# Kernel tuning notes

Hardware: AMD Instinct MI355X
Metric: run time of the kernel (lower is better)

The kernel has to match this reference:

```python
import jax, jax.numpy as jnp
import numpy as np
from jax import lax

BITS = 8
STRIDE = 1
PADDING = 1
SCALE = 2.0 ** (BITS - 1)  # fixed-point scale 2^(bits-1)


def setup_inputs() -> dict:
    key = jax.random.key(0)
    k1, k2, k3 = jax.random.split(key, 3)
    x = jax.random.normal(k1, (32, 128, 56, 56), dtype=jnp.float32)
    W = jax.random.normal(k2, (256, 128, 3, 3), dtype=jnp.float32)
    b = jax.random.normal(k3, (256,), dtype=jnp.float32)
    return {"x": x, "W": W, "b": b}


def reference(x, W, b):
    # to_fix_point: round(v * 2^(bits-1)); torch keeps long ints, but all
    # arithmetic in forward promotes back to float, so float round is exact here.
    w_q = jnp.round(W * SCALE)
    b_q = jnp.round(b * SCALE)
    # calConv: out[i,j] = sum(patch * w_q) / 2^(bits-1) + b_q
    # (square 3x3 kernel makes the original's transposed patch indexing a standard conv)
    out = lax.conv_general_dilated(
        x, w_q,
        window_strides=(STRIDE, STRIDE),
        padding=[(PADDING, PADDING), (PADDING, PADDING)],
        dimension_numbers=("NCHW", "OIHW", "NCHW"),
    )
    return out / SCALE + b_q[None, :, None, None]
```

## Files before the change

### kernel.cpp

```cpp
#include <hip/hip_runtime.h>

typedef _Float16 half8 __attribute__((ext_vector_type(8)));
typedef float floatx4 __attribute__((ext_vector_type(4)));

#define IMG   3136
#define PIMG  3364
#define XP_ELEMS (32 * 58 * 58 * 128)
#define WQ_ELEMS (9 * 256 * 128)

#define AS1 __attribute__((address_space(1)))
#define AS3 __attribute__((address_space(3)))

__global__ __launch_bounds__(256) void pad_x_kernel(const float* __restrict__ x,
                                                    _Float16* __restrict__ xp) {
    const int hh = blockIdx.x;
    const int n  = blockIdx.y;
    const int t  = threadIdx.x;
    _Float16* rowbase = xp + ((long)(n * 58 + hh) * 58) * 128;

    if (hh == 0 || hh == 57) {
        #pragma unroll
        for (int i = 0; i < 4; ++i) {
            int idx = i * 256 + t;
            if (idx < 928) *(half8*)(rowbase + idx * 8) = (half8)(_Float16)0.0f;
        }
        return;
    }

    __shared__ _Float16 tile[128 * 57];
    const int h = hh - 1;

    #pragma unroll
    for (int p = 0; p < 7; ++p) {
        int idx = p * 256 + t;
        int c   = idx / 14;
        int w4  = (idx % 14) * 4;
        const float4 v = *(const float4*)(x + ((long)(n * 128 + c) * 56 + h) * 56 + w4);
        _Float16* d = tile + c * 57 + w4;
        d[0] = (_Float16)v.x; d[1] = (_Float16)v.y;
        d[2] = (_Float16)v.z; d[3] = (_Float16)v.w;
    }
    __syncthreads();

    #pragma unroll
    for (int p = 0; p < 4; ++p) {
        int idx = p * 256 + t;
        if (idx < 896) {
            int ww = idx >> 4;
            int c0 = (idx & 15) * 8;
            half8 v;
            #pragma unroll
            for (int j = 0; j < 8; ++j) v[j] = tile[(c0 + j) * 57 + ww];
            *(half8*)(rowbase + (ww + 1) * 128 + c0) = v;
        }
    }
    if (t < 32) {
        int ww = (t >> 4) ? 57 : 0;
        int c0 = (t & 15) * 8;
        *(half8*)(rowbase + ww * 128 + c0) = (half8)(_Float16)0.0f;
    }
}

__global__ void quant_w_kernel(const float* __restrict__ W, _Float16* __restrict__ wq) {
    int t = blockIdx.x * 256 + threadIdx.x;
    int c  = t & 127;
    int k  = (t >> 7) & 255;
    int rs = t >> 15;
    wq[t] = (_Float16)rintf(W[(k * 128 + c) * 9 + rs] * 128.0f);
}

__global__ __launch_bounds__(256) void conv_mfma_kernel(
    const _Float16* __restrict__ xp, const _Float16* __restrict__ wq,
    const float* __restrict__ b, float* __restrict__ out)
{
    __shared__ __align__(16) _Float16 smem[24576];

    const int tid = threadIdx.x;
    const int l   = tid & 63;
    const int wv  = tid >> 6;
    const int wm  = wv & 1;
    const int wn  = wv >> 1;
    const int bx  = blockIdx.x;

    const int lrow = l >> 2;
    const int lch  = ((l & 3) ^ ((l >> 3) & 3)) * 8;

    int aoff[4];
    #pragma unroll
    for (int i = 0; i < 4; ++i)
        aoff[i] = (i * 64 + wv * 16 + lrow) * 128 + lch;

    int pb[2];
    #pragma unroll
    for (int j = 0; j < 2; ++j) {
        const int pix = bx * 128 + j * 64 + wv * 16 + lrow;
        const int n  = pix / IMG, hw = pix % IMG;
        pb[j] = (n * PIMG + (hw / 56) * 58 + (hw % 56)) * 128 + lch;
    }

    const int stA = wv * 512;

    floatx4 acc[8][4] = {};

    auto issue = [&](int t, int pbuf) {
        const int rs = t >> 2;
        const int cc = t & 3;
        const int r  = (rs * 11) >> 5;
        const int s2 = rs - r * 3;
        const _Float16* wg = wq + rs * (256 * 128) + cc * 32;
        const _Float16* xg = xp + (r * 58 + s2) * 128 + cc * 32;
        _Float16* A = smem + pbuf * 12288;
        _Float16* B = A + 8192;
        #pragma unroll
        for (int i = 0; i < 4; ++i)
            __builtin_amdgcn_global_load_lds((AS1 void*)(wg + aoff[i]),
                                             (AS3 void*)(A + i * 2048 + stA), 16, 0, 0);
        #pragma unroll
        for (int j = 0; j < 2; ++j)
            __builtin_amdgcn_global_load_lds((AS1 void*)(xg + pb[j]),
                                             (AS3 void*)(B + j * 2048 + stA), 16, 0, 0);
    };

    const int ar = wm * 128 + (l & 15);
    const int br = wn * 64 + (l & 15);
    const int kq = ((l >> 4) ^ ((l >> 1) & 3)) * 8;

    auto compute = [&](int pbuf) {
        const _Float16* As = smem + pbuf * 12288;
        const _Float16* Bs = As + 8192;
        half8 bf[4];
        #pragma unroll
        for (int ni = 0; ni < 4; ++ni)
            bf[ni] = *(const half8*)(Bs + (br + ni * 16) * 32 + kq);
        #pragma unroll
        for (int mi = 0; mi < 8; ++mi) {
            const half8 af = *(const half8*)(As + (ar + mi * 16) * 32 + kq);
            #pragma unroll
            for (int ni = 0; ni < 4; ++ni)
                acc[mi][ni] = __builtin_amdgcn_mfma_f32_16x16x32_f16(af, bf[ni], acc[mi][ni], 0, 0, 0);
        }
    };

    issue(0, 0);
    #pragma unroll 2
    for (int s = 0; s < 35; ++s) {
        issue(s + 1, (s + 1) & 1);
        asm volatile("s_waitcnt vmcnt(6)" ::: "memory");
        asm volatile("s_barrier" ::: "memory");
        compute(s & 1);
        asm volatile("s_barrier" ::: "memory");
    }
    asm volatile("s_waitcnt vmcnt(0)" ::: "memory");
    asm volatile("s_barrier" ::: "memory");
    compute(1);

    #pragma unroll
    for (int mi = 0; mi < 8; ++mi) {
        const int kb = wm * 128 + mi * 16 + (l >> 4) * 4;
        #pragma unroll
        for (int rg = 0; rg < 4; ++rg) {
            const int k = kb + rg;
            const float bq = rintf(b[k] * 128.0f);
            #pragma unroll
            for (int ni = 0; ni < 4; ++ni) {
                const int pix = bx * 128 + wn * 64 + ni * 16 + (l & 15);
                const int n  = pix / IMG;
                const int pr = pix - n * IMG;
                out[((long)n * 256 + k) * IMG + pr] = acc[mi][ni][rg] * (1.0f / 128.0f) + bq;
            }
        }
    }
}

__global__ void conv_fallback_kernel(const float* __restrict__ x, const float* __restrict__ W,
                                     const float* __restrict__ b, float* __restrict__ out)
{
    __shared__ float wsm[1152];
    const int k = blockIdx.y;
    for (int i = threadIdx.x; i < 1152; i += 256)
        wsm[i] = rintf(W[k * 1152 + i] * 128.0f);
    __syncthreads();
    const int pix = blockIdx.x * 256 + threadIdx.x;
    const int n = pix / IMG, hw = pix % IMG;
    const int h = hw / 56, w = hw % 56;
    float acc = 0.0f;
    for (int c = 0; c < 128; ++c) {
        const float* xr = x + ((n * 128 + c) * 56) * 56;
        const float* wr = wsm + c * 9;
        #pragma unroll
        for (int r = 0; r < 3; ++r) {
            const int hh = h + r - 1;
            if ((unsigned)hh >= 56u) continue;
            #pragma unroll
            for (int s = 0; s < 3; ++s) {
                const int ww = w + s - 1;
                if ((unsigned)ww >= 56u) continue;
                acc += xr[hh * 56 + ww] * wr[r * 3 + s];
            }
        }
    }
    out[((long)n * 256 + k) * IMG + hw] = acc * (1.0f / 128.0f) + rintf(b[k] * 128.0f);
}

extern "C" void kernel_launch(void* const* d_in, const int* in_sizes, int n_in,
                              void* d_out, int out_size, void* d_ws, size_t ws_size,
                              hipStream_t stream) {
    const float* x = (const float*)d_in[0];
    const float* W = (const float*)d_in[1];
    const float* b = (const float*)d_in[2];
    float* out = (float*)d_out;

    const size_t need = (size_t)XP_ELEMS * 2 + (size_t)WQ_ELEMS * 2;
    if (ws_size >= need) {
        _Float16* xp = (_Float16*)d_ws;
        _Float16* wq = xp + XP_ELEMS;
        pad_x_kernel<<<dim3(58, 32), 256, 0, stream>>>(x, xp);
        quant_w_kernel<<<WQ_ELEMS / 256, 256, 0, stream>>>(W, wq);
        conv_mfma_kernel<<<dim3(784), 256, 0, stream>>>(xp, wq, b, out);
    } else {
        conv_fallback_kernel<<<dim3(392, 256), 256, 0, stream>>>(x, W, b, out);
    }
}
```

Measured before the change: 206.9 us.

## Enlarge conv tile to 256x256 with 512 threads, K=64 stages, fused prep

Fuses padding and weight quantization into one prep kernel that also writes weights pre-swizzled in the staging layout. The conv kernel now uses 512-thread blocks covering 256 pixels per block with K-chunks of 64 channels (18 stages instead of 36). It spreads the next stage's loads between compute quads, raises wave priority around MFMA runs, and remaps block indices for locality. It aims to cut barrier and launch overhead and to improve reuse per load, at the cost of 128KB of LDS per block and fewer blocks (392).

```diff
diff --git a/kernel.cpp b/kernel.cpp
--- a/kernel.cpp
+++ b/kernel.cpp
@@ -11,11 +11,30 @@
 #define AS1 __attribute__((address_space(1)))
 #define AS3 __attribute__((address_space(3)))
 
-__global__ __launch_bounds__(256) void pad_x_kernel(const float* __restrict__ x,
-                                                    _Float16* __restrict__ xp) {
-    const int hh = blockIdx.x;
-    const int n  = blockIdx.y;
-    const int t  = threadIdx.x;
+__global__ __launch_bounds__(256) void prep_kernel(const float* __restrict__ x,
+                                                   const float* __restrict__ W,
+                                                   _Float16* __restrict__ xp,
+                                                   _Float16* __restrict__ wq) {
+    const int bid = blockIdx.x;
+    const int t   = threadIdx.x;
+    if (bid >= 1856) {
+        int U = (bid - 1856) * 256 + t;
+        int l  = U & 63;
+        int wv = (U >> 6) & 7;
+        int g  = (U >> 9) & 1;
+        int h  = (U >> 10) & 1;
+        int T  = U >> 11;
+        int rs = T >> 1, kt = T & 1;
+        int k  = h * 128 + g * 64 + wv * 8 + (l >> 3);
+        int c0 = kt * 64 + (((l & 7) ^ ((l >> 3) & 7)) * 8);
+        _Float16* d = wq + (long)U * 8;
+        #pragma unroll
+        for (int j = 0; j < 8; ++j)
+            d[j] = (_Float16)rintf(W[(k * 128 + c0 + j) * 9 + rs] * 128.0f);
+        return;
+    }
+    const int hh = bid % 58;
+    const int n  = bid / 58;
     _Float16* rowbase = xp + ((long)(n * 58 + hh) * 58) * 128;
 
     if (hh == 0 || hh == 57) {
@@ -61,98 +80,100 @@
     }
 }
 
-__global__ void quant_w_kernel(const float* __restrict__ W, _Float16* __restrict__ wq) {
-    int t = blockIdx.x * 256 + threadIdx.x;
-    int c  = t & 127;
-    int k  = (t >> 7) & 255;
-    int rs = t >> 15;
-    wq[t] = (_Float16)rintf(W[(k * 128 + c) * 9 + rs] * 128.0f);
-}
-
-__global__ __launch_bounds__(256) void conv_mfma_kernel(
+__global__ __launch_bounds__(512, 2) void conv_mfma_kernel(
     const _Float16* __restrict__ xp, const _Float16* __restrict__ wq,
     const float* __restrict__ b, float* __restrict__ out)
 {
-    __shared__ __align__(16) _Float16 smem[24576];
+    __shared__ __align__(16) _Float16 smem[65536];
 
     const int tid = threadIdx.x;
     const int l   = tid & 63;
     const int wv  = tid >> 6;
     const int wm  = wv & 1;
     const int wn  = wv >> 1;
-    const int bx  = blockIdx.x;
-
-    const int lrow = l >> 2;
-    const int lch  = ((l & 3) ^ ((l >> 3) & 3)) * 8;
-
-    int aoff[4];
-    #pragma unroll
-    for (int i = 0; i < 4; ++i)
-        aoff[i] = (i * 64 + wv * 16 + lrow) * 128 + lch;
-
-    int pb[2];
-    #pragma unroll
-    for (int j = 0; j < 2; ++j) {
-        const int pix = bx * 128 + j * 64 + wv * 16 + lrow;
-        const int n  = pix / IMG, hw = pix % IMG;
-        pb[j] = (n * PIMG + (hw / 56) * 58 + (hw % 56)) * 128 + lch;
-    }
-
-    const int stA = wv * 512;
+    int bx  = blockIdx.x;
+    bx = (bx & 7) * 49 + (bx >> 3);
+
+    const int lr3  = l >> 3;
+    const int l7   = l & 7;
+    const int l47  = l >> 4;
+    const int lswz = ((l & 7) ^ (lr3 & 7)) * 16;
+
+    long pbB[4];
+    #pragma unroll
+    for (int hg = 0; hg < 4; ++hg) {
+        const int pix = bx * 256 + hg * 64 + wv * 8 + lr3;
+        const int n = pix / IMG, hw = pix % IMG;
+        pbB[hg] = (long)(n * PIMG + (hw / 56) * 58 + (hw % 56)) * 256 + lswz;
+    }
+    const long abase = (long)wv * 1024 + l * 16;
 
     floatx4 acc[8][4] = {};
 
-    auto issue = [&](int t, int pbuf) {
-        const int rs = t >> 2;
-        const int cc = t & 3;
+    auto stageA = [&](int T, int h, int pbuf) {
+        const char* src = (const char*)wq + (long)((T * 2 + h) * 2) * 8192 + abase;
+        _Float16* dst = smem + pbuf * 32768 + (h * 128 + wv * 8) * 64;
+        __builtin_amdgcn_global_load_lds((AS1 void*)src,          (AS3 void*)dst,          16, 0, 0);
+        __builtin_amdgcn_global_load_lds((AS1 void*)(src + 8192), (AS3 void*)(dst + 4096), 16, 0, 0);
+    };
+    auto stageB = [&](int T, int h, int pbuf) {
+        const int rs = T >> 1, kt = T & 1;
         const int r  = (rs * 11) >> 5;
         const int s2 = rs - r * 3;
-        const _Float16* wg = wq + rs * (256 * 128) + cc * 32;
-        const _Float16* xg = xp + (r * 58 + s2) * 128 + cc * 32;
-        _Float16* A = smem + pbuf * 12288;
-        _Float16* B = A + 8192;
-        #pragma unroll
-        for (int i = 0; i < 4; ++i)
-            __builtin_amdgcn_global_load_lds((AS1 void*)(wg + aoff[i]),
-                                             (AS3 void*)(A + i * 2048 + stA), 16, 0, 0);
-        #pragma unroll
-        for (int j = 0; j < 2; ++j)
-            __builtin_amdgcn_global_load_lds((AS1 void*)(xg + pb[j]),
-                                             (AS3 void*)(B + j * 2048 + stA), 16, 0, 0);
+        const long toff = (long)(r * 58 + s2) * 256 + kt * 128;
+        const char* xb = (const char*)xp + toff;
+        _Float16* dst = smem + pbuf * 32768 + 16384 + (h * 128 + wv * 8) * 64;
+        __builtin_amdgcn_global_load_lds((AS1 void*)(xb + pbB[h * 2 + 0]), (AS3 void*)dst,          16, 0, 0);
+        __builtin_amdgcn_global_load_lds((AS1 void*)(xb + pbB[h * 2 + 1]), (AS3 void*)(dst + 4096), 16, 0, 0);
     };
 
-    const int ar = wm * 128 + (l & 15);
-    const int br = wn * 64 + (l & 15);
-    const int kq = ((l >> 4) ^ ((l >> 1) & 3)) * 8;
-
-    auto compute = [&](int pbuf) {
-        const _Float16* As = smem + pbuf * 12288;
-        const _Float16* Bs = As + 8192;
-        half8 bf[4];
-        #pragma unroll
-        for (int ni = 0; ni < 4; ++ni)
-            bf[ni] = *(const half8*)(Bs + (br + ni * 16) * 32 + kq);
-        #pragma unroll
-        for (int mi = 0; mi < 8; ++mi) {
-            const half8 af = *(const half8*)(As + (ar + mi * 16) * 32 + kq);
-            #pragma unroll
-            for (int ni = 0; ni < 4; ++ni)
-                acc[mi][ni] = __builtin_amdgcn_mfma_f32_16x16x32_f16(af, bf[ni], acc[mi][ni], 0, 0, 0);
-        }
-    };
-
-    issue(0, 0);
+    const int arow = wm * 128 + (l & 15);
+    const int brow = wn * 64 + (l & 15);
+
+    #define QUAD(q) { \
+        __builtin_amdgcn_s_setprio(1); \
+        _Pragma("unroll") for (int i = 0; i < 2; ++i) { \
+            const int mi = (q) * 2 + i; \
+            const half8 af0 = *(const half8*)(As + (arow + mi * 16) * 64 + ((0 + l47) ^ l7) * 8); \
+            const half8 af1 = *(const half8*)(As + (arow + mi * 16) * 64 + ((4 + l47) ^ l7) * 8); \
+            _Pragma("unroll") for (int ni = 0; ni < 4; ++ni) { \
+                acc[mi][ni] = __builtin_amdgcn_mfma_f32_16x16x32_f16(af0, bf[ni][0], acc[mi][ni], 0, 0, 0); \
+                acc[mi][ni] = __builtin_amdgcn_mfma_f32_16x16x32_f16(af1, bf[ni][1], acc[mi][ni], 0, 0, 0); \
+            } \
+        } \
+        __builtin_amdgcn_s_setprio(0); \
+    }
+
+    stageA(0, 0, 0); stageA(0, 1, 0); stageB(0, 0, 0); stageB(0, 1, 0);
+
     #pragma unroll 2
-    for (int s = 0; s < 35; ++s) {
-        issue(s + 1, (s + 1) & 1);
-        asm volatile("s_waitcnt vmcnt(6)" ::: "memory");
+    for (int T = 0; T < 18; ++T) {
+        const int pb = T & 1;
+        const _Float16* As = smem + pb * 32768;
+        const _Float16* Bs = As + 16384;
         asm volatile("s_barrier" ::: "memory");
-        compute(s & 1);
+        if (T < 17) {
+            stageA(T + 1, 0, pb ^ 1);
+            asm volatile("s_waitcnt vmcnt(2)" ::: "memory");
+        } else {
+            asm volatile("s_waitcnt vmcnt(0)" ::: "memory");
+        }
         asm volatile("s_barrier" ::: "memory");
-    }
-    asm volatile("s_waitcnt vmcnt(0)" ::: "memory");
-    asm volatile("s_barrier" ::: "memory");
-    compute(1);
+        half8 bf[4][2];
+        #pragma unroll
+        for (int ni = 0; ni < 4; ++ni) {
+            bf[ni][0] = *(const half8*)(Bs + (brow + ni * 16) * 64 + ((0 + l47) ^ l7) * 8);
+            bf[ni][1] = *(const half8*)(Bs + (brow + ni * 16) * 64 + ((4 + l47) ^ l7) * 8);
+        }
+        QUAD(0)
+        if (T < 17) stageA(T + 1, 1, pb ^ 1);
+        QUAD(1)
+        if (T < 17) stageB(T + 1, 0, pb ^ 1);
+        QUAD(2)
+        if (T < 17) stageB(T + 1, 1, pb ^ 1);
+        QUAD(3)
+    }
+    #undef QUAD
 
     #pragma unroll
     for (int mi = 0; mi < 8; ++mi) {
@@ -163,7 +184,7 @@
             const float bq = rintf(b[k] * 128.0f);
             #pragma unroll
             for (int ni = 0; ni < 4; ++ni) {
-                const int pix = bx * 128 + wn * 64 + ni * 16 + (l & 15);
+                const int pix = bx * 256 + wn * 64 + ni * 16 + (l & 15);
                 const int n  = pix / IMG;
                 const int pr = pix - n * IMG;
                 out[((long)n * 256 + k) * IMG + pr] = acc[mi][ni][rg] * (1.0f / 128.0f) + bq;
@@ -214,9 +235,8 @@
     if (ws_size >= need) {
         _Float16* xp = (_Float16*)d_ws;
         _Float16* wq = xp + XP_ELEMS;
-        pad_x_kernel<<<dim3(58, 32), 256, 0, stream>>>(x, xp);
-        quant_w_kernel<<<WQ_ELEMS / 256, 256, 0, stream>>>(W, wq);
-        conv_mfma_kernel<<<dim3(784), 256, 0, stream>>>(xp, wq, b, out);
+        prep_kernel<<<2000, 256, 0, stream>>>(x, W, xp, wq);
+        conv_mfma_kernel<<<dim3(392), 512, 0, stream>>>(xp, wq, b, out);
     } else {
         conv_fallback_kernel<<<dim3(392, 256), 256, 0, stream>>>(x, W, b, out);
     }
```

Result: no change. 204.4 us (-1.2%).
